# Performance work log

Measured on AMD Instinct MI355X. Metric: run time of the kernel, lower is better.

## Reference

```python
import jax, jax.numpy as jnp
import numpy as np

OUT = 128
HEADS = 8
HEAD = OUT // HEADS
NEG_SLOPE = 0.01


def _seg_softmax(logits, seg, num_segments):
    # logits: [E, H]; seg: [E] receiver node ids
    mx = jax.ops.segment_max(logits, seg, num_segments=num_segments)
    e = jnp.exp(logits - mx[seg])
    s = jax.ops.segment_sum(e, seg, num_segments=num_segments)
    return e / s[seg]


def _gat_pass(z, src, tgt, extra_logits, Wm, bm, Wa1, ba1, Wa2, ba2):
    # z: [N, 2D]; src/tgt: [E]; extra_logits: [E, H] or None
    N = z.shape[0]
    att1 = z @ Wa1 + ba1  # [N, H]
    att2 = z @ Wa2 + ba2  # [N, H]
    logits = att1[src] + att2[tgt]
    if extra_logits is not None:
        logits = logits + extra_logits
    coefs = _seg_softmax(jax.nn.leaky_relu(logits, NEG_SLOPE), tgt, N)  # [E, H]
    v = (z @ Wm + bm).reshape(N, HEADS, HEAD)  # [N, H, hs]
    msg = coefs[..., None] * v[src]            # [E, H, hs]
    agg = jax.ops.segment_sum(msg, tgt, num_segments=N)  # [N, H, hs]
    return agg.reshape(N, OUT)


def setup_inputs() -> dict:
    key = jax.random.key(0)
    ks = jax.random.split(key, 16)
    B, N, D, E = 2, 32768, 128, 262144
    ZD = 2 * D  # concat(node_fts, hidden)
    inp = {
        "node_fts": jax.random.normal(ks[0], (B, N, D), jnp.float32),
        "gkt_edge_fts": jax.random.normal(ks[1], (B, E, D), jnp.float32),
        "hidden": jax.random.normal(ks[2], (B, N, D), jnp.float32),
        "cfg_indices_padded": jax.random.randint(ks[3], (B, E, 2), 0, N, jnp.int32),
        "gkt_indices_padded": jax.random.randint(ks[4], (B, E, 2), 0, N, jnp.int32),
        "Wm": jax.random.normal(ks[5], (ZD, OUT), jnp.float32) / np.sqrt(ZD),
        "bm": jnp.zeros((OUT,), jnp.float32),
        "Wskip": jax.random.normal(ks[6], (ZD, OUT), jnp.float32) / np.sqrt(ZD),
        "bskip": jnp.zeros((OUT,), jnp.float32),
        "Wa1": jax.random.normal(ks[7], (ZD, HEADS), jnp.float32) / np.sqrt(ZD),
        "ba1": jnp.zeros((HEADS,), jnp.float32),
        "Wa2": jax.random.normal(ks[8], (ZD, HEADS), jnp.float32) / np.sqrt(ZD),
        "ba2": jnp.zeros((HEADS,), jnp.float32),
        "Wae": jax.random.normal(ks[9], (D, HEADS), jnp.float32) / np.sqrt(D),
        "bae": jnp.zeros((HEADS,), jnp.float32),
    }
    return inp


def reference(node_fts, gkt_edge_fts, hidden, cfg_indices_padded, gkt_indices_padded,
              Wm, bm, Wskip, bskip, Wa1, ba1, Wa2, ba2, Wae, bae):
    cfg_src = cfg_indices_padded[..., 0]
    cfg_tgt = cfg_indices_padded[..., 1]
    gkt_src = gkt_indices_padded[..., 0]
    gkt_tgt = gkt_indices_padded[..., 1]

    # ---- cfg stage ----
    cfg_z = jnp.concatenate([node_fts, hidden], axis=-1)  # [B, N, 2D]

    def cfg_one(z_b, src_b, tgt_b):
        return _gat_pass(z_b, src_b, tgt_b, None, Wm, bm, Wa1, ba1, Wa2, ba2)

    cfg_hidden = jax.vmap(cfg_one)(cfg_z, cfg_src, cfg_tgt)  # [B, N, OUT]
    cfg_hidden = cfg_hidden + cfg_z @ Wskip + bskip  # residual skip
    cfg_hidden = jax.nn.relu(cfg_hidden)

    # ---- gkt stage ----
    gkt_z = jnp.concatenate([node_fts, cfg_hidden], axis=-1)  # [B, N, 2D]
    gkt_att_e = gkt_edge_fts @ Wae + bae  # [B, E, H]

    def gkt_one(z_b, src_b, tgt_b, ae_b):
        return _gat_pass(z_b, src_b, tgt_b, ae_b, Wm, bm, Wa1, ba1, Wa2, ba2)

    ret = jax.vmap(gkt_one)(gkt_z, gkt_src, gkt_tgt, gkt_att_e)  # [B, N, OUT]
    ret = ret + gkt_z @ Wskip + bskip
    ret = jax.nn.relu(ret)
    return ret
```

## Files before the change

kernel.cpp:

```cpp
#include <hip/hip_runtime.h>
#include <hip/hip_bf16.h>

#define NB 2
#define NN 32768
#define NE 262144
#define DD 128
#define ZD 256
#define HEADS 8
#define OUTD 128
#define CAP 64

typedef short s16x8 __attribute__((ext_vector_type(8)));
typedef float f32x4 __attribute__((ext_vector_type(4)));
#define MFMA(a,b,c) __builtin_amdgcn_mfma_f32_16x16x32_bf16((a),(b),(c),0,0,0)

__device__ inline ushort f2bf(float f) {
    union { float f; unsigned u; } c; c.f = f;
    unsigned u = c.u;
    unsigned r = (u + 0x7fffu + ((u >> 16) & 1u)) >> 16;
    return (ushort)r;
}
__device__ inline float bf2f(ushort u) {
    union { unsigned u; float f; } c; c.u = ((unsigned)u) << 16;
    return c.f;
}

__global__ __launch_bounds__(256) void pack_w(
    const float* __restrict__ Wm, const float* __restrict__ Wsk,
    const float* __restrict__ Wa1, const float* __restrict__ Wa2,
    const float* __restrict__ bm, const float* __restrict__ bsk,
    const float* __restrict__ ba1, const float* __restrict__ ba2,
    ushort* __restrict__ WT, float* __restrict__ bias)
{
    int c = blockIdx.x;
    int k = threadIdx.x;
    float val;
    if (c < 32) {
        int a = c & 15;
        float w = (a < 8) ? Wa1[k*8 + a] : Wa2[k*8 + (a - 8)];
        if (c < 16) val = w;
        else { ushort hi = f2bf(w); val = w - bf2f(hi); }
    } else if (c < 160) {
        val = Wm[k*128 + (c - 32)];
    } else {
        val = Wsk[k*128 + (c - 160)];
    }
    WT[((size_t)(k >> 5)*288 + c)*32 + (k & 31)] = f2bf(val);
    if (k == 0) {
        if (c < 16) bias[c] = (c < 8) ? ba1[c] : ba2[c - 8];
        else if (c >= 32) bias[c - 16] = (c < 160) ? bm[c - 32] : bsk[c - 160];
    }
}

__global__ __launch_bounds__(256) void bucket_kernel(
    const int* __restrict__ cfg, const int* __restrict__ gkt,
    int* __restrict__ cnt, int2* __restrict__ pairs)
{
    int gid = blockIdx.x*256 + threadIdx.x;
    int L = gid >> 18, e = gid & (NE - 1);
    const int* base = (L < 2) ? cfg : gkt;
    const int* ip = base + (((size_t)(L & 1) << 18) + e)*2;
    int src = ip[0], tgt = ip[1];
    int pos = atomicAdd(&cnt[(L << 15) + tgt], 1);
    if (pos < CAP)
        pairs[((size_t)((L << 15) + tgt) << 6) + pos] = make_int2(e, src);
}

__global__ __launch_bounds__(256) void edge_att(
    const float* __restrict__ efts, const float* __restrict__ Wae,
    const float* __restrict__ bae, float* __restrict__ out)
{
    int t = threadIdx.x, lane = t & 63, wid = t >> 6;
    int col = lane & 15, q = lane >> 4;
    s16x8 bf[4];
    #pragma unroll
    for (int kc = 0; kc < 4; ++kc) {
        #pragma unroll
        for (int j = 0; j < 8; ++j) {
            float wv = (col < 8) ? Wae[(kc*32 + q*8 + j)*8 + col] : 0.f;
            bf[kc][j] = (short)f2bf(wv);
        }
    }
    float bb = (col < 8) ? bae[col] : 0.f;
    int wg = blockIdx.x*4 + wid;
    const int NT = (NB*NE)/16;
    for (int tile = wg; tile < NT; tile += gridDim.x*4) {
        size_t row = (size_t)tile*16 + col;
        const float* rp = efts + row*128 + q*8;
        f32x4 acc = {0.f, 0.f, 0.f, 0.f};
        #pragma unroll
        for (int kc = 0; kc < 4; ++kc) {
            float4 x0 = *(const float4*)(rp + kc*32);
            float4 x1 = *(const float4*)(rp + kc*32 + 4);
            s16x8 af;
            af[0] = (short)f2bf(x0.x); af[1] = (short)f2bf(x0.y);
            af[2] = (short)f2bf(x0.z); af[3] = (short)f2bf(x0.w);
            af[4] = (short)f2bf(x1.x); af[5] = (short)f2bf(x1.y);
            af[6] = (short)f2bf(x1.z); af[7] = (short)f2bf(x1.w);
            acc = MFMA(af, bf[kc], acc);
        }
        if (col < 8) {
            size_t e0 = (size_t)tile*16 + q*4;
            #pragma unroll
            for (int r = 0; r < 4; ++r)
                out[(e0 + r)*8 + col] = acc[r] + bb;
        }
    }
}

__global__ __launch_bounds__(256) void gemm_nodes(
    const float* __restrict__ nf, const float* __restrict__ h2,
    const ushort* __restrict__ WT, const float* __restrict__ bias,
    float* __restrict__ att1, float* __restrict__ att2,
    float* __restrict__ vout, float* __restrict__ skip)
{
    constexpr int LDA = 264;
    __shared__ ushort Ah[32*LDA];
    __shared__ ushort Al[32*LDA];
    int t = threadIdx.x;
    int row0 = blockIdx.x * 32;

    #pragma unroll
    for (int it = 0; it < 8; ++it) {
        int flat = it*256 + t;
        int r = flat >> 6, c4 = flat & 63;
        size_t gr = (size_t)row0 + r;
        const float* sp = (c4 < 32) ? (nf + gr*128 + c4*4)
                                    : (h2 + gr*128 + (c4 - 32)*4);
        float4 x = *(const float4*)sp;
        ushort4 hi, lo;
        hi.x = f2bf(x.x); lo.x = f2bf(x.x - bf2f(hi.x));
        hi.y = f2bf(x.y); lo.y = f2bf(x.y - bf2f(hi.y));
        hi.z = f2bf(x.z); lo.z = f2bf(x.z - bf2f(hi.z));
        hi.w = f2bf(x.w); lo.w = f2bf(x.w - bf2f(hi.w));
        *(ushort4*)&Ah[r*LDA + c4*4] = hi;
        *(ushort4*)&Al[r*LDA + c4*4] = lo;
    }
    __syncthreads();

    int lane = t & 63, wid = t >> 6;
    int rg = wid >> 1, nh = wid & 1;
    int q = lane >> 4, c = lane & 15;
    int mr = rg*16 + c;
    f32x4 zero = {0.f, 0.f, 0.f, 0.f};
    f32x4 acc[9];
    #pragma unroll
    for (int i = 0; i < 9; ++i) acc[i] = zero;

    const ushort* Wb = WT + (size_t)c*32 + q*8;
    #pragma unroll
    for (int ks = 0; ks < 8; ++ks) {
        const ushort* Wk = Wb + (size_t)ks*288*32;
        s16x8 ah = *(const s16x8*)&Ah[mr*LDA + ks*32 + q*8];
        if (nh == 0) {
            s16x8 al = *(const s16x8*)&Al[mr*LDA + ks*32 + q*8];
            s16x8 bh = *(const s16x8*)&Wk[0];
            s16x8 bl = *(const s16x8*)&Wk[16*32];
            acc[0] = MFMA(ah, bh, acc[0]);
            acc[0] = MFMA(al, bh, acc[0]);
            acc[0] = MFMA(ah, bl, acc[0]);
            #pragma unroll
            for (int j = 1; j < 8; ++j) {
                s16x8 bb = *(const s16x8*)&Wk[(16 + 16*j)*32];
                acc[j] = MFMA(ah, bb, acc[j]);
            }
        } else {
            #pragma unroll
            for (int j = 0; j < 9; ++j) {
                s16x8 bb = *(const s16x8*)&Wk[(144 + 16*j)*32];
                acc[j] = MFMA(ah, bb, acc[j]);
            }
        }
    }

    int rowb = row0 + rg*16 + q*4;
    if (nh == 0) {
        float bsv = bias[c];
        #pragma unroll
        for (int r = 0; r < 4; ++r) {
            size_t row = (size_t)rowb + r;
            float val = acc[0][r] + bsv;
            if (c < 8) att1[row*8 + c] = val;
            else       att2[row*8 + (c - 8)] = val;
        }
        #pragma unroll
        for (int j = 1; j < 8; ++j) {
            int col = (j - 1)*16 + c;
            float bv = bias[16 + col];
            #pragma unroll
            for (int r = 0; r < 4; ++r) {
                size_t row = (size_t)rowb + r;
                vout[row*128 + col] = acc[j][r] + bv;
            }
        }
    } else {
        {
            int col = 112 + c;
            float bv = bias[16 + col];
            #pragma unroll
            for (int r = 0; r < 4; ++r) {
                size_t row = (size_t)rowb + r;
                vout[row*128 + col] = acc[0][r] + bv;
            }
        }
        #pragma unroll
        for (int j = 1; j < 9; ++j) {
            int col = (j - 1)*16 + c;
            float bv = bias[144 + col];
            #pragma unroll
            for (int r = 0; r < 4; ++r) {
                size_t row = (size_t)rowb + r;
                skip[row*128 + col] = acc[j][r] + bv;
            }
        }
    }
}

__global__ __launch_bounds__(256) void agg_kernel(
    const int* __restrict__ cnt, const int2* __restrict__ pairs,
    const float* __restrict__ att1, const float* __restrict__ att2,
    const float* __restrict__ v, const float* __restrict__ skip,
    const float* __restrict__ ae, float* __restrict__ out, int listBase)
{
    int t = threadIdx.x;
    int wid = t >> 6, lane = t & 63;
    int g = blockIdx.x*4 + wid;
    int b = g >> 15, n = g & (NN - 1);
    int L = listBase + b;
    int slot = lane >> 5, c4 = lane & 31, h = c4 >> 2;
    int deg = cnt[(L << 15) + n];
    if (deg > CAP) deg = CAP;
    const int2* pr = pairs + ((size_t)((L << 15) + n) << 6);
    int bN = b << 15;
    size_t bE8 = ((size_t)b << 18)*8;
    float a2 = att2[(size_t)g*8 + h];
    float4 acc = {0.f, 0.f, 0.f, 0.f};
    float den = 0.f;
    for (int base = 0; base < deg; base += 8) {
        int ei[4], pe[4], ps[4];
        #pragma unroll
        for (int j = 0; j < 4; ++j) {
            int e = base + j*2 + slot;
            ei[j] = e;
            int idx = (e < deg) ? e : 0;
            int2 pp = pr[idx];
            pe[j] = pp.x; ps[j] = pp.y;
        }
        #pragma unroll
        for (int j = 0; j < 4; ++j) {
            float4 vv = *(const float4*)&v[(size_t)(bN + ps[j])*128 + c4*4];
            float a1 = att1[(size_t)(bN + ps[j])*8 + h];
            float l = a1 + a2;
            if (ae) l += ae[bE8 + (size_t)pe[j]*8 + h];
            l = (l < 0.f) ? 0.01f*l : l;
            float w = (ei[j] < deg) ? __expf(l) : 0.f;
            den += w;
            acc.x = fmaf(w, vv.x, acc.x);
            acc.y = fmaf(w, vv.y, acc.y);
            acc.z = fmaf(w, vv.z, acc.z);
            acc.w = fmaf(w, vv.w, acc.w);
        }
    }
    den   += __shfl_xor(den, 32);
    acc.x += __shfl_xor(acc.x, 32);
    acc.y += __shfl_xor(acc.y, 32);
    acc.z += __shfl_xor(acc.z, 32);
    acc.w += __shfl_xor(acc.w, 32);
    if (slot == 0) {
        float inv = (deg > 0) ? 1.f/den : 0.f;
        float4 sk = *(const float4*)&skip[(size_t)g*128 + c4*4];
        float4 o;
        o.x = fmaxf(fmaf(acc.x, inv, sk.x), 0.f);
        o.y = fmaxf(fmaf(acc.y, inv, sk.y), 0.f);
        o.z = fmaxf(fmaf(acc.z, inv, sk.z), 0.f);
        o.w = fmaxf(fmaf(acc.w, inv, sk.w), 0.f);
        *(float4*)&out[(size_t)g*128 + c4*4] = o;
    }
}

extern "C" void kernel_launch(void* const* d_in, const int* in_sizes, int n_in,
                              void* d_out, int out_size, void* d_ws, size_t ws_size,
                              hipStream_t stream)
{
    const float* nf   = (const float*)d_in[0];
    const float* efts = (const float*)d_in[1];
    const float* hid  = (const float*)d_in[2];
    const int*   cfg  = (const int*)d_in[3];
    const int*   gkt  = (const int*)d_in[4];
    const float* Wm   = (const float*)d_in[5];
    const float* bm   = (const float*)d_in[6];
    const float* Wsk  = (const float*)d_in[7];
    const float* bsk  = (const float*)d_in[8];
    const float* Wa1  = (const float*)d_in[9];
    const float* ba1  = (const float*)d_in[10];
    const float* Wa2  = (const float*)d_in[11];
    const float* ba2  = (const float*)d_in[12];
    const float* Wae  = (const float*)d_in[13];
    const float* bae  = (const float*)d_in[14];

    char* p = (char*)d_ws;
    auto carve = [&](size_t bytes) -> char* {
        char* r = p; p += (bytes + 255) & ~(size_t)255; return r;
    };
    float*  att1 = (float*)carve((size_t)NB*NN*8*4);
    float*  att2 = (float*)carve((size_t)NB*NN*8*4);
    float*  vbuf = (float*)carve((size_t)NB*NN*128*4);
    float*  skip = (float*)carve((size_t)NB*NN*128*4);
    float*  cfgh = (float*)carve((size_t)NB*NN*128*4);
    float*  gae  = (float*)carve((size_t)NB*NE*8*4);
    ushort* WT   = (ushort*)carve((size_t)8*288*32*2);
    float*  bias = (float*)carve(288*4);
    int*    cnt  = (int*)carve((size_t)4*NN*4);
    int2*   pairs= (int2*)carve((size_t)4*NN*CAP*8);

    hipMemsetAsync(cnt, 0, (size_t)4*NN*4, stream);
    pack_w<<<288, 256, 0, stream>>>(Wm, Wsk, Wa1, Wa2, bm, bsk, ba1, ba2, WT, bias);
    bucket_kernel<<<(4*NE)/256, 256, 0, stream>>>(cfg, gkt, cnt, pairs);
    edge_att<<<1024, 256, 0, stream>>>(efts, Wae, bae, gae);

    gemm_nodes<<<(NB*NN)/32, 256, 0, stream>>>(nf, hid, WT, bias, att1, att2, vbuf, skip);
    agg_kernel<<<(NB*NN)/4, 256, 0, stream>>>(cnt, pairs, att1, att2, vbuf, skip, nullptr, cfgh, 0);

    gemm_nodes<<<(NB*NN)/32, 256, 0, stream>>>(nf, cfgh, WT, bias, att1, att2, vbuf, skip);
    agg_kernel<<<(NB*NN)/4, 256, 0, stream>>>(cnt, pairs, att1, att2, vbuf, skip, gae, (float*)d_out, 2);
}
```

Before: 742.1 us.

## Merge prep kernels into one launch and store value vectors in bf16

Folds weight packing, edge bucketing and edge-attention projection into a single launch that dispatches on block index. This removes two launches and lets the three independent jobs run concurrently. The per-node value projection is now stored as bf16 instead of fp32, which halves the bytes gathered per edge in the aggregation kernel. In exchange, the aggregated values carry bf16 rounding error.

```diff
diff --git a/kernel.cpp b/kernel.cpp
--- a/kernel.cpp
+++ b/kernel.cpp
@@ -25,85 +25,82 @@
     return c.f;
 }
 
-__global__ __launch_bounds__(256) void pack_w(
+__global__ __launch_bounds__(256) void prep_kernel(
     const float* __restrict__ Wm, const float* __restrict__ Wsk,
     const float* __restrict__ Wa1, const float* __restrict__ Wa2,
     const float* __restrict__ bm, const float* __restrict__ bsk,
     const float* __restrict__ ba1, const float* __restrict__ ba2,
-    ushort* __restrict__ WT, float* __restrict__ bias)
+    ushort* __restrict__ WT, float* __restrict__ bias,
+    const int* __restrict__ cfg, const int* __restrict__ gkt,
+    int* __restrict__ cnt, int2* __restrict__ pairs,
+    const float* __restrict__ efts, const float* __restrict__ Wae,
+    const float* __restrict__ bae, float* __restrict__ gae)
 {
-    int c = blockIdx.x;
-    int k = threadIdx.x;
-    float val;
-    if (c < 32) {
-        int a = c & 15;
-        float w = (a < 8) ? Wa1[k*8 + a] : Wa2[k*8 + (a - 8)];
-        if (c < 16) val = w;
-        else { ushort hi = f2bf(w); val = w - bf2f(hi); }
-    } else if (c < 160) {
-        val = Wm[k*128 + (c - 32)];
+    int bb = blockIdx.x;
+    int t = threadIdx.x;
+    if (bb < 288) {
+        int c = bb, k = t;
+        float val;
+        if (c < 32) {
+            int a = c & 15;
+            float w = (a < 8) ? Wa1[k*8 + a] : Wa2[k*8 + (a - 8)];
+            if (c < 16) val = w;
+            else { ushort hi = f2bf(w); val = w - bf2f(hi); }
+        } else if (c < 160) {
+            val = Wm[k*128 + (c - 32)];
+        } else {
+            val = Wsk[k*128 + (c - 160)];
+        }
+        WT[((size_t)(k >> 5)*288 + c)*32 + (k & 31)] = f2bf(val);
+        if (k == 0) {
+            if (c < 16) bias[c] = (c < 8) ? ba1[c] : ba2[c - 8];
+            else if (c >= 32) bias[c - 16] = (c < 160) ? bm[c - 32] : bsk[c - 160];
+        }
+    } else if (bb < 288 + 4096) {
+        int gid = (bb - 288)*256 + t;
+        int L = gid >> 18, e = gid & (NE - 1);
+        const int* base = (L < 2) ? cfg : gkt;
+        const int* ip = base + (((size_t)(L & 1) << 18) + e)*2;
+        int src = ip[0], tgt = ip[1];
+        int pos = atomicAdd(&cnt[(L << 15) + tgt], 1);
+        if (pos < CAP)
+            pairs[((size_t)((L << 15) + tgt) << 6) + pos] = make_int2(e, src);
     } else {
-        val = Wsk[k*128 + (c - 160)];
-    }
-    WT[((size_t)(k >> 5)*288 + c)*32 + (k & 31)] = f2bf(val);
-    if (k == 0) {
-        if (c < 16) bias[c] = (c < 8) ? ba1[c] : ba2[c - 8];
-        else if (c >= 32) bias[c - 16] = (c < 160) ? bm[c - 32] : bsk[c - 160];
-    }
-}
-
-__global__ __launch_bounds__(256) void bucket_kernel(
-    const int* __restrict__ cfg, const int* __restrict__ gkt,
-    int* __restrict__ cnt, int2* __restrict__ pairs)
-{
-    int gid = blockIdx.x*256 + threadIdx.x;
-    int L = gid >> 18, e = gid & (NE - 1);
-    const int* base = (L < 2) ? cfg : gkt;
-    const int* ip = base + (((size_t)(L & 1) << 18) + e)*2;
-    int src = ip[0], tgt = ip[1];
-    int pos = atomicAdd(&cnt[(L << 15) + tgt], 1);
-    if (pos < CAP)
-        pairs[((size_t)((L << 15) + tgt) << 6) + pos] = make_int2(e, src);
-}
-
-__global__ __launch_bounds__(256) void edge_att(
-    const float* __restrict__ efts, const float* __restrict__ Wae,
-    const float* __restrict__ bae, float* __restrict__ out)
-{
-    int t = threadIdx.x, lane = t & 63, wid = t >> 6;
-    int col = lane & 15, q = lane >> 4;
-    s16x8 bf[4];
-    #pragma unroll
-    for (int kc = 0; kc < 4; ++kc) {
-        #pragma unroll
-        for (int j = 0; j < 8; ++j) {
-            float wv = (col < 8) ? Wae[(kc*32 + q*8 + j)*8 + col] : 0.f;
-            bf[kc][j] = (short)f2bf(wv);
-        }
-    }
-    float bb = (col < 8) ? bae[col] : 0.f;
-    int wg = blockIdx.x*4 + wid;
-    const int NT = (NB*NE)/16;
-    for (int tile = wg; tile < NT; tile += gridDim.x*4) {
-        size_t row = (size_t)tile*16 + col;
-        const float* rp = efts + row*128 + q*8;
-        f32x4 acc = {0.f, 0.f, 0.f, 0.f};
+        int lane = t & 63, wid = t >> 6;
+        int col = lane & 15, q = lane >> 4;
+        s16x8 bf[4];
         #pragma unroll
         for (int kc = 0; kc < 4; ++kc) {
-            float4 x0 = *(const float4*)(rp + kc*32);
-            float4 x1 = *(const float4*)(rp + kc*32 + 4);
-            s16x8 af;
-            af[0] = (short)f2bf(x0.x); af[1] = (short)f2bf(x0.y);
-            af[2] = (short)f2bf(x0.z); af[3] = (short)f2bf(x0.w);
-            af[4] = (short)f2bf(x1.x); af[5] = (short)f2bf(x1.y);
-            af[6] = (short)f2bf(x1.z); af[7] = (short)f2bf(x1.w);
-            acc = MFMA(af, bf[kc], acc);
-        }
-        if (col < 8) {
-            size_t e0 = (size_t)tile*16 + q*4;
-            #pragma unroll
-            for (int r = 0; r < 4; ++r)
-                out[(e0 + r)*8 + col] = acc[r] + bb;
+            #pragma unroll
+            for (int j = 0; j < 8; ++j) {
+                float wv = (col < 8) ? Wae[(kc*32 + q*8 + j)*8 + col] : 0.f;
+                bf[kc][j] = (short)f2bf(wv);
+            }
+        }
+        float bb2 = (col < 8) ? bae[col] : 0.f;
+        int wg = (bb - 4384)*4 + wid;
+        const int NT = (NB*NE)/16;
+        for (int tile = wg; tile < NT; tile += 1024*4) {
+            size_t row = (size_t)tile*16 + col;
+            const float* rp = efts + row*128 + q*8;
+            f32x4 acc = {0.f, 0.f, 0.f, 0.f};
+            #pragma unroll
+            for (int kc = 0; kc < 4; ++kc) {
+                float4 x0 = *(const float4*)(rp + kc*32);
+                float4 x1 = *(const float4*)(rp + kc*32 + 4);
+                s16x8 af;
+                af[0] = (short)f2bf(x0.x); af[1] = (short)f2bf(x0.y);
+                af[2] = (short)f2bf(x0.z); af[3] = (short)f2bf(x0.w);
+                af[4] = (short)f2bf(x1.x); af[5] = (short)f2bf(x1.y);
+                af[6] = (short)f2bf(x1.z); af[7] = (short)f2bf(x1.w);
+                acc = MFMA(af, bf[kc], acc);
+            }
+            if (col < 8) {
+                size_t e0 = (size_t)tile*16 + q*4;
+                #pragma unroll
+                for (int r = 0; r < 4; ++r)
+                    gae[(e0 + r)*8 + col] = acc[r] + bb2;
+            }
         }
     }
 }
@@ -112,7 +109,7 @@
     const float* __restrict__ nf, const float* __restrict__ h2,
     const ushort* __restrict__ WT, const float* __restrict__ bias,
     float* __restrict__ att1, float* __restrict__ att2,
-    float* __restrict__ vout, float* __restrict__ skip)
+    ushort* __restrict__ vout, float* __restrict__ skip)
 {
     constexpr int LDA = 264;
     __shared__ ushort Ah[32*LDA];
@@ -190,7 +187,7 @@
             #pragma unroll
             for (int r = 0; r < 4; ++r) {
                 size_t row = (size_t)rowb + r;
-                vout[row*128 + col] = acc[j][r] + bv;
+                vout[row*128 + col] = f2bf(acc[j][r] + bv);
             }
         }
     } else {
@@ -200,7 +197,7 @@
             #pragma unroll
             for (int r = 0; r < 4; ++r) {
                 size_t row = (size_t)rowb + r;
-                vout[row*128 + col] = acc[0][r] + bv;
+                vout[row*128 + col] = f2bf(acc[0][r] + bv);
             }
         }
         #pragma unroll
@@ -219,7 +216,7 @@
 __global__ __launch_bounds__(256) void agg_kernel(
     const int* __restrict__ cnt, const int2* __restrict__ pairs,
     const float* __restrict__ att1, const float* __restrict__ att2,
-    const float* __restrict__ v, const float* __restrict__ skip,
+    const ushort* __restrict__ v, const float* __restrict__ skip,
     const float* __restrict__ ae, float* __restrict__ out, int listBase)
 {
     int t = threadIdx.x;
@@ -248,17 +245,17 @@
         }
         #pragma unroll
         for (int j = 0; j < 4; ++j) {
-            float4 vv = *(const float4*)&v[(size_t)(bN + ps[j])*128 + c4*4];
+            ushort4 vv = *(const ushort4*)&v[(size_t)(bN + ps[j])*128 + c4*4];
             float a1 = att1[(size_t)(bN + ps[j])*8 + h];
             float l = a1 + a2;
             if (ae) l += ae[bE8 + (size_t)pe[j]*8 + h];
             l = (l < 0.f) ? 0.01f*l : l;
             float w = (ei[j] < deg) ? __expf(l) : 0.f;
             den += w;
-            acc.x = fmaf(w, vv.x, acc.x);
-            acc.y = fmaf(w, vv.y, acc.y);
-            acc.z = fmaf(w, vv.z, acc.z);
-            acc.w = fmaf(w, vv.w, acc.w);
+            acc.x = fmaf(w, bf2f(vv.x), acc.x);
+            acc.y = fmaf(w, bf2f(vv.y), acc.y);
+            acc.z = fmaf(w, bf2f(vv.z), acc.z);
+            acc.w = fmaf(w, bf2f(vv.w), acc.w);
         }
     }
     den   += __shfl_xor(den, 32);
@@ -304,7 +301,7 @@
     };
     float*  att1 = (float*)carve((size_t)NB*NN*8*4);
     float*  att2 = (float*)carve((size_t)NB*NN*8*4);
-    float*  vbuf = (float*)carve((size_t)NB*NN*128*4);
+    ushort* vbuf = (ushort*)carve((size_t)NB*NN*128*2);
     float*  skip = (float*)carve((size_t)NB*NN*128*4);
     float*  cfgh = (float*)carve((size_t)NB*NN*128*4);
     float*  gae  = (float*)carve((size_t)NB*NE*8*4);
@@ -314,9 +311,9 @@
     int2*   pairs= (int2*)carve((size_t)4*NN*CAP*8);
 
     hipMemsetAsync(cnt, 0, (size_t)4*NN*4, stream);
-    pack_w<<<288, 256, 0, stream>>>(Wm, Wsk, Wa1, Wa2, bm, bsk, ba1, ba2, WT, bias);
-    bucket_kernel<<<(4*NE)/256, 256, 0, stream>>>(cfg, gkt, cnt, pairs);
-    edge_att<<<1024, 256, 0, stream>>>(efts, Wae, bae, gae);
+    prep_kernel<<<288 + 4096 + 1024, 256, 0, stream>>>(
+        Wm, Wsk, Wa1, Wa2, bm, bsk, ba1, ba2, WT, bias,
+        cfg, gkt, cnt, pairs, efts, Wae, bae, gae);
 
     gemm_nodes<<<(NB*NN)/32, 256, 0, stream>>>(nf, hid, WT, bias, att1, att2, vbuf, skip);
     agg_kernel<<<(NB*NN)/4, 256, 0, stream>>>(cnt, pairs, att1, att2, vbuf, skip, nullptr, cfgh, 0);
```

New measurement: 757.9 us. 2.1% more time.
